# Performance work log

Measured on AMD Instinct MI355X. Metric: run time of the kernel, lower is better.

The kernel has to match this reference:

```python
import jax, jax.numpy as jnp
import numpy as np

D, M, B = 4096, 1024, 64

def build_tile_idx(D, b):
    T = D // (2 * b)
    d4 = D // 4
    hb = b // 2
    t = np.arange(T)
    # horizontal tiles: view x as (D/4, 4); rows t*hb..(t+1)*hb, cols 0..3
    rows = t[:, None, None] * hb + np.arange(hb)[None, :, None]          # (T, hb, 1)
    horiz = (rows * 4 + np.arange(4)[None, None, :]).reshape(T, -1)      # (T, 2b)
    # vertical tiles: view x as (4, D/4); rows 0..3, cols t*hb..(t+1)*hb
    cols = t[:, None, None] * hb + np.arange(hb)[None, None, :]          # (T, 1, hb)
    vert = (np.arange(4)[None, :, None] * d4 + cols).reshape(T, -1)      # (T, 2b)
    return np.concatenate([horiz, vert], axis=0)                          # (G=2T, 2b)

def setup_inputs() -> dict:
    key = jax.random.key(0)
    k1, k2 = jax.random.split(key)
    N = 2048
    T = D // (2 * B)
    G = 2 * T
    e = M // G                     # experts per group
    tile_size = 2 * B
    x_flat = jax.random.normal(k1, (N, D), dtype=jnp.float32)
    V = jax.random.normal(k2, (G, e, tile_size, B), dtype=jnp.float32)
    tile_idx = jnp.asarray(build_tile_idx(D, B), dtype=jnp.int32)
    return {"x_flat": x_flat, "V": V, "tile_idx": tile_idx}

def reference(x_flat, V, tile_idx):
    # UnitColNorm(dim=2): normalize V columns along the tile_size axis
    Vn = V / jnp.linalg.norm(V, axis=2, keepdims=True)
    # gather tiles: (N, G, tile_size)
    x_tiles = x_flat[:, tile_idx]
    # grouped batched matmul: (N,G,t) x (G,e,t,b) -> (N,G,e,b)
    h = jnp.einsum('ngt,getb->ngeb', x_tiles, Vn)
    N = x_flat.shape[0]
    return h.reshape(N, M, B)
```

## Files before the change

kernel.cpp:

```cpp
#include <hip/hip_runtime.h>
#include <hip/hip_bf16.h>

typedef short s16x8 __attribute__((ext_vector_type(8)));
typedef float f32x16 __attribute__((ext_vector_type(16)));

#define D_DIM 4096
#define OUT_STRIDE 65536

__device__ __forceinline__ unsigned int f2bf(float f) {
    unsigned int u = __float_as_uint(f);
    u += 0x7FFFu + ((u >> 16) & 1u);
    return u >> 16;
}
__device__ __forceinline__ unsigned int pk2(float a, float b) {
    return f2bf(a) | (f2bf(b) << 16);
}

__global__ __launch_bounds__(256) void vnorm_kernel(const float* __restrict__ V,
                                                    unsigned short* __restrict__ Bn) {
    const int blk = blockIdx.x;
    const int tid = threadIdx.x;
    const float* Vt = V + (size_t)blk * 8192;
    __shared__ float tile[8192];
    __shared__ float part[256];
    __shared__ float rnorm[64];

    for (int i = tid; i < 2048; i += 256)
        ((float4*)tile)[i] = ((const float4*)Vt)[i];
    __syncthreads();

    {
        int b = tid & 63, q = tid >> 6;
        float s = 0.f;
        for (int t = q; t < 128; t += 4) { float v = tile[t * 64 + b]; s += v * v; }
        part[tid] = s;
    }
    __syncthreads();
    if (tid < 64) {
        float tot = part[tid] + part[tid + 64] + part[tid + 128] + part[tid + 192];
        rnorm[tid] = rsqrtf(tot);
    }
    __syncthreads();

    unsigned short* rowbase = Bn + (size_t)blk * 64 * 128;
    for (int iter = 0; iter < 4; ++iter) {
        int idx = iter * 256 + tid;
        int b = idx >> 4, k8 = idx & 15;
        float rn = rnorm[b];
        unsigned int w[4];
        int tb = k8 * 8;
        #pragma unroll
        for (int j = 0; j < 4; ++j) {
            float v0 = tile[(tb + 2 * j) * 64 + b] * rn;
            float v1 = tile[(tb + 2 * j + 1) * 64 + b] * rn;
            w[j] = pk2(v0, v1);
        }
        uint4* dst = (uint4*)(rowbase + b * 128) + k8;
        *dst = make_uint4(w[0], w[1], w[2], w[3]);
    }
}

__global__ __launch_bounds__(1024, 4) void gemm_kernel(const float* __restrict__ x,
                                                       const unsigned short* __restrict__ Bn,
                                                       float* __restrict__ out) {
    const int g = blockIdx.x;
    const int m0 = blockIdx.y * 128;
    const int tid = threadIdx.x;
    const int lane = tid & 63, wv = tid >> 6;
    const int jl = lane & 31, hi = lane >> 5;

    __shared__ __align__(16) unsigned short Alds[16384];

    s16x8 bfrag[2][8];
    {
        const char* Bbase = (const char*)(Bn + (size_t)g * 131072);
        #pragma unroll
        for (int nf = 0; nf < 2; ++nf) {
            const char* rb = Bbase + (wv * 64 + nf * 32 + jl) * 256 + hi * 16;
            #pragma unroll
            for (int ks = 0; ks < 8; ++ks)
                bfrag[nf][ks] = *(const s16x8*)(rb + ks * 32);
        }
    }

    #pragma unroll
    for (int p = 0; p < 2; ++p) {
        int c = tid + p * 1024;
        int r = c >> 4, kc = c & 15;
        int k0 = kc * 8;
        int idx = (g < 32) ? (g * 128 + k0)
                           : ((k0 >> 5) * 1024 + (g - 32) * 32 + (k0 & 31));
        const float* xp = x + (size_t)(m0 + r) * D_DIM + idx;
        float4 v0 = *(const float4*)xp;
        float4 v1 = *(const float4*)(xp + 4);
        uint4 w = make_uint4(pk2(v0.x, v0.y), pk2(v0.z, v0.w),
                             pk2(v1.x, v1.y), pk2(v1.z, v1.w));
        *(uint4*)((char*)Alds + r * 256 + ((kc * 16) ^ ((r & 7) << 4))) = w;
    }
    __syncthreads();

    const int swz = (jl & 7) << 4;
    #pragma unroll
    for (int rs = 0; rs < 4; ++rs) {
        const char* Ab = (const char*)Alds + (rs * 32 + jl) * 256;
        f32x16 acc0 = {0.f}, acc1 = {0.f};
        #pragma unroll
        for (int ks = 0; ks < 8; ++ks) {
            s16x8 a = *(const s16x8*)(Ab + ((ks * 32 + hi * 16) ^ swz));
            acc0 = __builtin_amdgcn_mfma_f32_32x32x16_bf16(a, bfrag[0][ks], acc0, 0, 0, 0);
            acc1 = __builtin_amdgcn_mfma_f32_32x32x16_bf16(a, bfrag[1][ks], acc1, 0, 0, 0);
        }
        float* obase = out + (size_t)(m0 + rs * 32 + 4 * hi) * OUT_STRIDE
                     + g * 1024 + wv * 64 + jl;
        #pragma unroll
        for (int reg = 0; reg < 16; ++reg) {
            int row = (reg & 3) + 8 * (reg >> 2);
            float* p = obase + (size_t)row * OUT_STRIDE;
            __builtin_nontemporal_store(acc0[reg], p);
            __builtin_nontemporal_store(acc1[reg], p + 32);
        }
    }
}

extern "C" void kernel_launch(void* const* d_in, const int* in_sizes, int n_in,
                              void* d_out, int out_size, void* d_ws, size_t ws_size,
                              hipStream_t stream) {
    const float* x = (const float*)d_in[0];
    const float* V = (const float*)d_in[1];
    float* out = (float*)d_out;
    unsigned short* Bn = (unsigned short*)d_ws;

    const int N = in_sizes[0] / D_DIM;
    const int nmt = N / 128;

    vnorm_kernel<<<1024, 256, 0, stream>>>(V, Bn);
    gemm_kernel<<<dim3(64, nmt), 1024, 0, stream>>>(x, Bn, out);
}
```

Measured before the change: 146.5 us.

## Loop each GEMM block over four M chunks with double-buffered A staging

Each GEMM workgroup now handles 512 rows of x instead of 128. It loads the B fragments for its group once and reuses them across four 128-row chunks. The A tile for the next chunk is staged into a second LDS buffer while the current chunk's MFMAs and stores run. The grid shrinks from 64x16 to 4x64 blocks, so there are fewer workgroups to cover the 256 CUs, and LDS use per block doubles.

```diff
diff --git a/kernel.cpp b/kernel.cpp
--- a/kernel.cpp
+++ b/kernel.cpp
@@ -63,13 +63,14 @@
 __global__ __launch_bounds__(1024, 4) void gemm_kernel(const float* __restrict__ x,
                                                        const unsigned short* __restrict__ Bn,
                                                        float* __restrict__ out) {
-    const int g = blockIdx.x;
-    const int m0 = blockIdx.y * 128;
+    const int s = blockIdx.x;
+    const int g = blockIdx.y;
     const int tid = threadIdx.x;
     const int lane = tid & 63, wv = tid >> 6;
     const int jl = lane & 31, hi = lane >> 5;
+    const int m_base = s * 512;
 
-    __shared__ __align__(16) unsigned short Alds[16384];
+    __shared__ __align__(16) unsigned short Alds[2][16384];
 
     s16x8 bfrag[2][8];
     {
@@ -83,43 +84,57 @@
         }
     }
 
+    const int swz = (jl & 7) << 4;
+
+    #define STAGE(MC, BUF)                                                        \
+        {                                                                         \
+            _Pragma("unroll")                                                     \
+            for (int p = 0; p < 2; ++p) {                                         \
+                int c = tid + p * 1024;                                           \
+                int r = c >> 4, kc = c & 15;                                      \
+                int k0 = kc * 8;                                                  \
+                int idx = (g < 32) ? (g * 128 + k0)                               \
+                                   : ((k0 >> 5) * 1024 + (g - 32) * 32 + (k0 & 31)); \
+                const float* xp = x + (size_t)(m_base + (MC) * 128 + r) * D_DIM + idx; \
+                float4 v0 = *(const float4*)xp;                                   \
+                float4 v1 = *(const float4*)(xp + 4);                             \
+                uint4 w = make_uint4(pk2(v0.x, v0.y), pk2(v0.z, v0.w),            \
+                                     pk2(v1.x, v1.y), pk2(v1.z, v1.w));           \
+                *(uint4*)((char*)Alds[BUF] + r * 256 + ((kc * 16) ^ ((r & 7) << 4))) = w; \
+            }                                                                     \
+        }
+
+    STAGE(0, 0);
+
     #pragma unroll
-    for (int p = 0; p < 2; ++p) {
-        int c = tid + p * 1024;
-        int r = c >> 4, kc = c & 15;
-        int k0 = kc * 8;
-        int idx = (g < 32) ? (g * 128 + k0)
-                           : ((k0 >> 5) * 1024 + (g - 32) * 32 + (k0 & 31));
-        const float* xp = x + (size_t)(m0 + r) * D_DIM + idx;
-        float4 v0 = *(const float4*)xp;
-        float4 v1 = *(const float4*)(xp + 4);
-        uint4 w = make_uint4(pk2(v0.x, v0.y), pk2(v0.z, v0.w),
-                             pk2(v1.x, v1.y), pk2(v1.z, v1.w));
-        *(uint4*)((char*)Alds + r * 256 + ((kc * 16) ^ ((r & 7) << 4))) = w;
-    }
-    __syncthreads();
+    for (int mc = 0; mc < 4; ++mc) {
+        __syncthreads();
+        if (mc < 3) STAGE(mc + 1, (mc + 1) & 1);
 
-    const int swz = (jl & 7) << 4;
-    #pragma unroll
-    for (int rs = 0; rs < 4; ++rs) {
-        const char* Ab = (const char*)Alds + (rs * 32 + jl) * 256;
-        f32x16 acc0 = {0.f}, acc1 = {0.f};
+        const char* Acur = (const char*)Alds[mc & 1];
+        const int m0 = m_base + mc * 128;
         #pragma unroll
-        for (int ks = 0; ks < 8; ++ks) {
-            s16x8 a = *(const s16x8*)(Ab + ((ks * 32 + hi * 16) ^ swz));
-            acc0 = __builtin_amdgcn_mfma_f32_32x32x16_bf16(a, bfrag[0][ks], acc0, 0, 0, 0);
-            acc1 = __builtin_amdgcn_mfma_f32_32x32x16_bf16(a, bfrag[1][ks], acc1, 0, 0, 0);
-        }
-        float* obase = out + (size_t)(m0 + rs * 32 + 4 * hi) * OUT_STRIDE
-                     + g * 1024 + wv * 64 + jl;
-        #pragma unroll
-        for (int reg = 0; reg < 16; ++reg) {
-            int row = (reg & 3) + 8 * (reg >> 2);
-            float* p = obase + (size_t)row * OUT_STRIDE;
-            __builtin_nontemporal_store(acc0[reg], p);
-            __builtin_nontemporal_store(acc1[reg], p + 32);
+        for (int rs = 0; rs < 4; ++rs) {
+            const char* Ab = Acur + (rs * 32 + jl) * 256;
+            f32x16 acc0 = {0.f}, acc1 = {0.f};
+            #pragma unroll
+            for (int ks = 0; ks < 8; ++ks) {
+                s16x8 a = *(const s16x8*)(Ab + ((ks * 32 + hi * 16) ^ swz));
+                acc0 = __builtin_amdgcn_mfma_f32_32x32x16_bf16(a, bfrag[0][ks], acc0, 0, 0, 0);
+                acc1 = __builtin_amdgcn_mfma_f32_32x32x16_bf16(a, bfrag[1][ks], acc1, 0, 0, 0);
+            }
+            float* obase = out + (size_t)(m0 + rs * 32 + 4 * hi) * OUT_STRIDE
+                         + g * 1024 + wv * 64 + jl;
+            #pragma unroll
+            for (int reg = 0; reg < 16; ++reg) {
+                int row = (reg & 3) + 8 * (reg >> 2);
+                float* p = obase + (size_t)row * OUT_STRIDE;
+                __builtin_nontemporal_store(acc0[reg], p);
+                __builtin_nontemporal_store(acc1[reg], p + 32);
+            }
         }
     }
+    #undef STAGE
 }
 
 extern "C" void kernel_launch(void* const* d_in, const int* in_sizes, int n_in,
@@ -131,8 +146,8 @@
     unsigned short* Bn = (unsigned short*)d_ws;
 
     const int N = in_sizes[0] / D_DIM;
-    const int nmt = N / 128;
+    const int nsplit = N / 512;
 
     vnorm_kernel<<<1024, 256, 0, stream>>>(V, Bn);
-    gemm_kernel<<<dim3(64, nmt), 1024, 0, stream>>>(x, Bn, out);
+    gemm_kernel<<<dim3(nsplit, 64), 1024, 0, stream>>>(x, Bn, out);
 }
```

Measured after the change: 141.1 us. -3.7%, faster.
